# Optimization experiments

Hardware: AMD Instinct MI355X
Metric: run time of the kernel (lower is better)

The kernel has to match this reference:

```python
import jax, jax.numpy as jnp
import numpy as np

N_NODES = 50000
N_EDGES = 800000
H = 64      # node_hidden_size
S = 16      # static_feature_size
EF = 16     # edge_feature_size
ATT_IN = 2 * H + 2 * S + EF   # 176
ATT_W = 2 * H + EF            # 144
UPD_IN = 2 * H                # 128
UPD_W = 2 * H                 # 128


def setup_inputs() -> dict:
    key = jax.random.key(0)
    ks = jax.random.split(key, 12)
    x = jax.random.normal(ks[0], (N_NODES, H), dtype=jnp.float32)
    x_s = jax.random.normal(ks[1], (N_NODES, S), dtype=jnp.float32)
    edge_index = jax.random.randint(ks[2], (2, N_EDGES), 0, N_NODES, dtype=jnp.int32)
    edge_features = jax.random.normal(ks[3], (N_EDGES, EF), dtype=jnp.float32)

    def lin(k, out_dim, in_dim):
        lim = 1.0 / np.sqrt(in_dim)
        kw, kb = jax.random.split(k)
        W = jax.random.uniform(kw, (out_dim, in_dim), minval=-lim, maxval=lim, dtype=jnp.float32)
        b = jax.random.uniform(kb, (out_dim,), minval=-lim, maxval=lim, dtype=jnp.float32)
        return W, b

    att_w1, att_b1 = lin(ks[4], ATT_W, ATT_IN)
    att_w2, att_b2 = lin(ks[5], 1, ATT_W)
    upd_w1, upd_b1 = lin(ks[6], UPD_W, UPD_IN)
    upd_w2, upd_b2 = lin(ks[7], H, UPD_W)

    return {
        "x": x, "x_s": x_s, "edge_index": edge_index, "edge_features": edge_features,
        "att_w1": att_w1, "att_b1": att_b1, "att_w2": att_w2, "att_b2": att_b2,
        "upd_w1": upd_w1, "upd_b1": upd_b1, "upd_w2": upd_w2, "upd_b2": upd_b2,
    }


def segment_softmax(scores, segment_ids, num_segments):
    max_scores = jax.ops.segment_max(scores, segment_ids, num_segments=num_segments)
    exp_scores = jnp.exp(scores - max_scores[segment_ids])
    sum_exp = jax.ops.segment_sum(exp_scores, segment_ids, num_segments=num_segments)
    return exp_scores / (sum_exp[segment_ids] + 1e-9)


def reference(x, x_s, edge_index, edge_features,
              att_w1, att_b1, att_w2, att_b2,
              upd_w1, upd_b1, upd_w2, upd_b2):
    num_nodes = x.shape[0]
    src, dst = edge_index[0], edge_index[1]

    # gather per-edge features: [E, 2H+2S+EF]
    att_in = jnp.concatenate(
        [x[src], x[dst], x_s[src], x_s[dst], edge_features], axis=-1)

    # attention MLP (depth=1, relu hidden), squeeze to [E]
    h = jax.nn.relu(att_in @ att_w1.T + att_b1)
    raw = (h @ att_w2.T + att_b2).squeeze(-1)
    raw = jax.nn.leaky_relu(raw)

    attn = segment_softmax(raw, dst, num_nodes)

    # weighted scatter-sum of source hidden feats -> [N, H]
    aggregated = jax.ops.segment_sum(x[src] * attn[:, None], dst, num_segments=num_nodes)

    upd_in = jnp.concatenate([x, aggregated], axis=-1)
    u = jax.nn.relu(upd_in @ upd_w1.T + upd_b1)
    out = u @ upd_w2.T + upd_b2
    return jax.nn.relu(out)
```

## Files before the change

### kernel.cpp

```cpp
#include <hip/hip_runtime.h>
#include <math.h>

#define N_NODES_C 50000
#define E_C       800000
#define ATT_IN_C  176
#define ATT_HID_C 144
#define SCAN_B    98
#define UPD_TILES 3125

typedef __attribute__((ext_vector_type(8))) __bf16 bf16x8;
typedef __attribute__((ext_vector_type(4))) float f32x4;

#define O_RAW   0L
#define O_DEG   3201024L
#define O_OFF   3402752L
#define O_CUR   3603456L
#define O_CSR   3804160L
#define O_EFB   16605184L
#define O_XB    42206208L
#define O_XSB   48607232L
#define O_W1B   50208256L
#define O_UW1B  50259968L
#define O_UW2B  50293760L
#define O_AGGB  50311168L
#define O_PSUM  O_AGGB
#define O_BOFF  (O_AGGB + 512L)

__device__ __forceinline__ bf16x8 bzero8() {
    bf16x8 z;
#pragma unroll
    for (int i = 0; i < 8; ++i) z[i] = (__bf16)0.0f;
    return z;
}

__global__ __launch_bounds__(256) void k_deg(const int* __restrict__ ei, int* __restrict__ deg) {
    int e = blockIdx.x * blockDim.x + threadIdx.x;
    if (e < E_C) atomicAdd(&deg[ei[E_C + e]], 1);
}

__global__ __launch_bounds__(256) void k_scan1(const int* __restrict__ deg,
                                               int* __restrict__ psum) {
    __shared__ int red[256];
    int b = blockIdx.x, t = threadIdx.x;
    int i = b * 512 + t * 2;
    int s = 0;
    if (i < N_NODES_C) s += deg[i];
    if (i + 1 < N_NODES_C) s += deg[i + 1];
    red[t] = s;
    __syncthreads();
#pragma unroll
    for (int off = 128; off > 0; off >>= 1) {
        if (t < off) red[t] += red[t + off];
        __syncthreads();
    }
    if (t == 0) psum[b] = red[0];
}

__global__ __launch_bounds__(128) void k_scan2(const int* __restrict__ psum,
                                               int* __restrict__ boff,
                                               int* __restrict__ offsets) {
    __shared__ int sc[128];
    int t = threadIdx.x;
    int v = (t < SCAN_B) ? psum[t] : 0;
    sc[t] = v;
    __syncthreads();
#pragma unroll
    for (int off = 1; off < 128; off <<= 1) {
        int val = sc[t];
        int add = (t >= off) ? sc[t - off] : 0;
        __syncthreads();
        sc[t] = val + add;
        __syncthreads();
    }
    boff[t] = sc[t] - v;
    if (t == SCAN_B - 1) offsets[N_NODES_C] = sc[t];
}

__global__ __launch_bounds__(256) void k_scan3(const int* __restrict__ deg,
                                               const int* __restrict__ boff,
                                               int* __restrict__ offsets,
                                               int* __restrict__ cursor) {
    __shared__ int sc[256];
    int b = blockIdx.x, t = threadIdx.x;
    int i = b * 512 + t * 2;
    int d0 = (i < N_NODES_C) ? deg[i] : 0;
    int d1 = (i + 1 < N_NODES_C) ? deg[i + 1] : 0;
    int s = d0 + d1;
    sc[t] = s;
    __syncthreads();
#pragma unroll
    for (int off = 1; off < 256; off <<= 1) {
        int val = sc[t];
        int add = (t >= off) ? sc[t - off] : 0;
        __syncthreads();
        sc[t] = val + add;
        __syncthreads();
    }
    int excl = boff[b] + sc[t] - s;
    if (i < N_NODES_C)     { offsets[i]     = excl;      cursor[i]     = excl; }
    if (i + 1 < N_NODES_C) { offsets[i + 1] = excl + d0; cursor[i + 1] = excl + d0; }
}

__global__ __launch_bounds__(256) void k_fill(const int* __restrict__ ei,
                                              int* __restrict__ cursor,
                                              int4* __restrict__ csr) {
    int e = blockIdx.x * blockDim.x + threadIdx.x;
    if (e < E_C) {
        int src  = ei[e];
        int dst  = ei[E_C + e];
        int slot = atomicAdd(&cursor[dst], 1);
        csr[slot] = make_int4(src, dst, e, 0);
    }
}

__global__ __launch_bounds__(256) void k_cvt(
    const float* __restrict__ x, const float* __restrict__ xs,
    const float* __restrict__ ef, const float* __restrict__ w1,
    const float* __restrict__ uw1, const float* __restrict__ uw2,
    __bf16* __restrict__ xb, __bf16* __restrict__ xsb,
    __bf16* __restrict__ efb, __bf16* __restrict__ w1b,
    __bf16* __restrict__ uw1b, __bf16* __restrict__ uw2b)
{
    long g = (long)blockIdx.x * 256 + threadIdx.x;
    const long G_X = 400000, G_XS = 500000, G_EF = 2100000,
               G_W1 = 2103168, G_UW1 = 2105216, G_UW2 = 2106240;
    if (g >= G_UW2) return;
    const float* src; __bf16* dst; long off;
    if (g < G_X)        { src = x;   dst = xb;   off = g * 8; }
    else if (g < G_XS)  { src = xs;  dst = xsb;  off = (g - G_X) * 8; }
    else if (g < G_EF)  { src = ef;  dst = efb;  off = (g - G_XS) * 8; }
    else if (g < G_W1)  { src = w1;  dst = w1b;  off = (g - G_EF) * 8; }
    else if (g < G_UW1) { src = uw1; dst = uw1b; off = (g - G_W1) * 8; }
    else                { src = uw2; dst = uw2b; off = (g - G_UW1) * 8; }
    float4 a = *(const float4*)(src + off);
    float4 b = *(const float4*)(src + off + 4);
    bf16x8 o;
    o[0] = (__bf16)a.x; o[1] = (__bf16)a.y; o[2] = (__bf16)a.z; o[3] = (__bf16)a.w;
    o[4] = (__bf16)b.x; o[5] = (__bf16)b.y; o[6] = (__bf16)b.z; o[7] = (__bf16)b.w;
    *(bf16x8*)(dst + off) = o;
}

__device__ __forceinline__ void load_afrags(
    int src, int dst, int e, int quad,
    const __bf16* __restrict__ xb, const __bf16* __restrict__ xsb,
    const __bf16* __restrict__ efb,
    bf16x8 a[6])
{
    const __bf16* px = xb + (long)src * 64 + quad * 8;
    const __bf16* pd = xb + (long)dst * 64 + quad * 8;
    a[0] = *(const bf16x8*)(px);
    a[1] = *(const bf16x8*)(px + 32);
    a[2] = *(const bf16x8*)(pd);
    a[3] = *(const bf16x8*)(pd + 32);
    if (quad < 2) {
        a[4] = *(const bf16x8*)(xsb + (long)src * 16 + quad * 8);
        a[5] = *(const bf16x8*)(efb + (long)e * 16 + quad * 8);
    } else {
        a[4] = *(const bf16x8*)(xsb + (long)dst * 16 + (quad - 2) * 8);
        a[5] = bzero8();
    }
}

__global__ __launch_bounds__(256) void k_scores_mfma(
    const __bf16* __restrict__ xb, const __bf16* __restrict__ xsb,
    const __bf16* __restrict__ efb, const __bf16* __restrict__ w1b,
    const int4* __restrict__ csr,
    const float* __restrict__ b1, const float* __restrict__ w2,
    const float* __restrict__ b2, float* __restrict__ raw)
{
    int tid  = threadIdx.x;
    int lane = tid & 63;
    int w    = blockIdx.x * 4 + (tid >> 6);
    const int NP = E_C / 32;
    int per = (NP + 1023) / 1024;
    long j0 = (long)w * per;
    long j1 = j0 + per; if (j1 > NP) j1 = NP;
    if (j0 >= j1) return;

    int mrow = lane & 15;
    int quad = lane >> 4;

    bf16x8 bfr[6][9];
#pragma unroll
    for (int ks = 0; ks < 6; ++ks) {
        int k0 = ks * 32 + quad * 8;
#pragma unroll
        for (int nt = 0; nt < 9; ++nt) {
            int n = nt * 16 + mrow;
            if (k0 + 8 <= ATT_IN_C)
                bfr[ks][nt] = *(const bf16x8*)(w1b + (long)n * ATT_IN_C + k0);
            else
                bfr[ks][nt] = bzero8();
        }
    }

    float b1v[9], w2v[9];
#pragma unroll
    for (int nt = 0; nt < 9; ++nt) {
        int n = nt * 16 + mrow;
        b1v[nt] = b1[n];
        w2v[nt] = w2[n];
    }
    float b2v = b2[0];

    bf16x8 curA[6], curB[6], nxtA[6], nxtB[6];
    int4 cA = make_int4(0, 0, 0, 0), cB = cA;
    {
        int4 e0 = csr[j0 * 32 + mrow];
        int4 e1 = csr[j0 * 32 + 16 + mrow];
        load_afrags(e0.x, e0.y, e0.z, quad, xb, xsb, efb, curA);
        load_afrags(e1.x, e1.y, e1.z, quad, xb, xsb, efb, curB);
        if (j0 + 1 < j1) {
            int4 f0 = csr[(j0 + 1) * 32 + mrow];
            int4 f1 = csr[(j0 + 1) * 32 + 16 + mrow];
            load_afrags(f0.x, f0.y, f0.z, quad, xb, xsb, efb, nxtA);
            load_afrags(f1.x, f1.y, f1.z, quad, xb, xsb, efb, nxtB);
        }
    }

    for (long j = j0; j < j1; ++j) {
        if (j + 2 < j1) {
            cA = csr[(j + 2) * 32 + mrow];
            cB = csr[(j + 2) * 32 + 16 + mrow];
        }

        f32x4 accA[9], accB[9];
#pragma unroll
        for (int nt = 0; nt < 9; ++nt) {
            accA[nt] = (f32x4){0.f, 0.f, 0.f, 0.f};
            accB[nt] = (f32x4){0.f, 0.f, 0.f, 0.f};
        }

#pragma unroll
        for (int ks = 0; ks < 6; ++ks) {
#pragma unroll
            for (int nt = 0; nt < 9; ++nt) {
                accA[nt] = __builtin_amdgcn_mfma_f32_16x16x32_bf16(
                    curA[ks], bfr[ks][nt], accA[nt], 0, 0, 0);
                accB[nt] = __builtin_amdgcn_mfma_f32_16x16x32_bf16(
                    curB[ks], bfr[ks][nt], accB[nt], 0, 0, 0);
            }
        }

        float pA0 = 0.f, pA1 = 0.f, pA2 = 0.f, pA3 = 0.f;
        float pB0 = 0.f, pB1 = 0.f, pB2 = 0.f, pB3 = 0.f;
#pragma unroll
        for (int nt = 0; nt < 9; ++nt) {
            pA0 += w2v[nt] * fmaxf(accA[nt][0] + b1v[nt], 0.f);
            pA1 += w2v[nt] * fmaxf(accA[nt][1] + b1v[nt], 0.f);
            pA2 += w2v[nt] * fmaxf(accA[nt][2] + b1v[nt], 0.f);
            pA3 += w2v[nt] * fmaxf(accA[nt][3] + b1v[nt], 0.f);
            pB0 += w2v[nt] * fmaxf(accB[nt][0] + b1v[nt], 0.f);
            pB1 += w2v[nt] * fmaxf(accB[nt][1] + b1v[nt], 0.f);
            pB2 += w2v[nt] * fmaxf(accB[nt][2] + b1v[nt], 0.f);
            pB3 += w2v[nt] * fmaxf(accB[nt][3] + b1v[nt], 0.f);
        }
#pragma unroll
        for (int off = 1; off < 16; off <<= 1) {
            pA0 += __shfl_xor(pA0, off, 64);
            pA1 += __shfl_xor(pA1, off, 64);
            pA2 += __shfl_xor(pA2, off, 64);
            pA3 += __shfl_xor(pA3, off, 64);
            pB0 += __shfl_xor(pB0, off, 64);
            pB1 += __shfl_xor(pB1, off, 64);
            pB2 += __shfl_xor(pB2, off, 64);
            pB3 += __shfl_xor(pB3, off, 64);
        }
        if (mrow < 4) {
            float vA = (mrow == 0) ? pA0 : (mrow == 1) ? pA1 : (mrow == 2) ? pA2 : pA3;
            float vB = (mrow == 0) ? pB0 : (mrow == 1) ? pB1 : (mrow == 2) ? pB2 : pB3;
            vA += b2v; vB += b2v;
            vA = (vA >= 0.f) ? vA : 0.01f * vA;
            vB = (vB >= 0.f) ? vB : 0.01f * vB;
            raw[(j * 2) * 16 + quad * 4 + mrow]     = vA;
            raw[(j * 2 + 1) * 16 + quad * 4 + mrow] = vB;
        }

#pragma unroll
        for (int i = 0; i < 6; ++i) { curA[i] = nxtA[i]; curB[i] = nxtB[i]; }
        if (j + 2 < j1) {
            load_afrags(cA.x, cA.y, cA.z, quad, xb, xsb, efb, nxtA);
            load_afrags(cB.x, cB.y, cB.z, quad, xb, xsb, efb, nxtB);
        }
    }
}

__global__ __launch_bounds__(256) void k_agg(
    const __bf16* __restrict__ xb, const int* __restrict__ offsets,
    const int4* __restrict__ csr,
    const float* __restrict__ raw, __bf16* __restrict__ aggb)
{
    int tid = threadIdx.x;
    int wave = tid >> 6, lane = tid & 63;
    int v = blockIdx.x * 4 + wave;
    if (v >= N_NODES_C) return;
    int s0 = offsets[v], s1 = offsets[v + 1];

    float m = -INFINITY;
    for (int p = s0 + lane; p < s1; p += 64) m = fmaxf(m, raw[p]);
#pragma unroll
    for (int off = 32; off > 0; off >>= 1) m = fmaxf(m, __shfl_xor(m, off, 64));

    float acc = 0.f, sum = 0.f;
    for (int p = s0; p < s1; ++p) {
        int src = csr[p].x;
        float w = expf(raw[p] - m);
        sum += w;
        acc += w * (float)xb[(long)src * 64 + lane];
    }
    aggb[(long)v * 64 + lane] = (__bf16)(acc / (sum + 1e-9f));
}

__global__ __launch_bounds__(256) void k_upd_mfma(
    const __bf16* __restrict__ xb, const __bf16* __restrict__ aggb,
    const __bf16* __restrict__ w1b, const float* __restrict__ b1,
    const __bf16* __restrict__ w2b, const float* __restrict__ b2,
    float* __restrict__ out)
{
    __shared__ __bf16 ubuf[4][16 * 136];
    int tid = threadIdx.x, wid = tid >> 6, lane = tid & 63;
    int tile = blockIdx.x * 4 + wid;
    if (tile >= UPD_TILES) return;
    int mrow = lane & 15, quad = lane >> 4;

    long node = (long)tile * 16 + mrow;
    bf16x8 a1[4];
    a1[0] = *(const bf16x8*)(xb + node * 64 + quad * 8);
    a1[1] = *(const bf16x8*)(xb + node * 64 + 32 + quad * 8);
    a1[2] = *(const bf16x8*)(aggb + node * 64 + quad * 8);
    a1[3] = *(const bf16x8*)(aggb + node * 64 + 32 + quad * 8);

    bf16x8 b1f[4][8];
#pragma unroll
    for (int ks = 0; ks < 4; ++ks)
#pragma unroll
        for (int nt = 0; nt < 8; ++nt)
            b1f[ks][nt] = *(const bf16x8*)(w1b + (long)(nt * 16 + mrow) * 128 + ks * 32 + quad * 8);

    f32x4 acc1[8];
#pragma unroll
    for (int nt = 0; nt < 8; ++nt) acc1[nt] = (f32x4){0.f, 0.f, 0.f, 0.f};
#pragma unroll
    for (int ks = 0; ks < 4; ++ks)
#pragma unroll
        for (int nt = 0; nt < 8; ++nt)
            acc1[nt] = __builtin_amdgcn_mfma_f32_16x16x32_bf16(a1[ks], b1f[ks][nt], acc1[nt], 0, 0, 0);

    __bf16* ub = ubuf[wid];
#pragma unroll
    for (int nt = 0; nt < 8; ++nt) {
        float bb = b1[nt * 16 + mrow];
#pragma unroll
        for (int r = 0; r < 4; ++r) {
            float h = fmaxf(acc1[nt][r] + bb, 0.f);
            ub[(quad * 4 + r) * 136 + nt * 16 + mrow] = (__bf16)h;
        }
    }

    bf16x8 a2[4];
#pragma unroll
    for (int ks = 0; ks < 4; ++ks)
        a2[ks] = *(bf16x8*)&ub[mrow * 136 + ks * 32 + quad * 8];

    bf16x8 b2f[4][4];
#pragma unroll
    for (int ks = 0; ks < 4; ++ks)
#pragma unroll
        for (int nt = 0; nt < 4; ++nt)
            b2f[ks][nt] = *(const bf16x8*)(w2b + (long)(nt * 16 + mrow) * 128 + ks * 32 + quad * 8);

    f32x4 acc2[4];
#pragma unroll
    for (int nt = 0; nt < 4; ++nt) acc2[nt] = (f32x4){0.f, 0.f, 0.f, 0.f};
#pragma unroll
    for (int ks = 0; ks < 4; ++ks)
#pragma unroll
        for (int nt = 0; nt < 4; ++nt)
            acc2[nt] = __builtin_amdgcn_mfma_f32_16x16x32_bf16(a2[ks], b2f[ks][nt], acc2[nt], 0, 0, 0);

#pragma unroll
    for (int nt = 0; nt < 4; ++nt) {
        float bb = b2[nt * 16 + mrow];
#pragma unroll
        for (int r = 0; r < 4; ++r) {
            long nodeo = (long)tile * 16 + quad * 4 + r;
            out[nodeo * 64 + nt * 16 + mrow] = fmaxf(acc2[nt][r] + bb, 0.f);
        }
    }
}

extern "C" void kernel_launch(void* const* d_in, const int* in_sizes, int n_in,
                              void* d_out, int out_size, void* d_ws, size_t ws_size,
                              hipStream_t stream) {
    const float* x    = (const float*)d_in[0];
    const float* xs   = (const float*)d_in[1];
    const int*   ei   = (const int*)d_in[2];
    const float* ef   = (const float*)d_in[3];
    const float* aw1  = (const float*)d_in[4];
    const float* ab1  = (const float*)d_in[5];
    const float* aw2  = (const float*)d_in[6];
    const float* ab2  = (const float*)d_in[7];
    const float* uw1  = (const float*)d_in[8];
    const float* ub1  = (const float*)d_in[9];
    const float* uw2  = (const float*)d_in[10];
    const float* ub2  = (const float*)d_in[11];
    float* out = (float*)d_out;

    char* ws = (char*)d_ws;
    float*  raw     = (float*)(ws + O_RAW);
    int*    deg     = (int*)(ws + O_DEG);
    int*    offsets = (int*)(ws + O_OFF);
    int*    cursor  = (int*)(ws + O_CUR);
    int4*   csr     = (int4*)(ws + O_CSR);
    __bf16* efb     = (__bf16*)(ws + O_EFB);
    __bf16* xb      = (__bf16*)(ws + O_XB);
    __bf16* xsb     = (__bf16*)(ws + O_XSB);
    __bf16* w1b     = (__bf16*)(ws + O_W1B);
    __bf16* uw1b    = (__bf16*)(ws + O_UW1B);
    __bf16* uw2b    = (__bf16*)(ws + O_UW2B);
    __bf16* aggb    = (__bf16*)(ws + O_AGGB);
    int*    psum    = (int*)(ws + O_PSUM);
    int*    boff    = (int*)(ws + O_BOFF);

    hipMemsetAsync(deg, 0, N_NODES_C * sizeof(int), stream);
    hipLaunchKernelGGL(k_deg,      dim3((E_C + 255) / 256),       dim3(256), 0, stream, ei, deg);
    hipLaunchKernelGGL(k_scan1,    dim3(SCAN_B),                  dim3(256), 0, stream, deg, psum);
    hipLaunchKernelGGL(k_scan2,    dim3(1),                       dim3(128), 0, stream, psum, boff, offsets);
    hipLaunchKernelGGL(k_scan3,    dim3(SCAN_B),                  dim3(256), 0, stream, deg, boff, offsets, cursor);
    hipLaunchKernelGGL(k_fill,     dim3((E_C + 255) / 256),       dim3(256), 0, stream,
                       ei, cursor, csr);
    hipLaunchKernelGGL(k_cvt,      dim3(8228),                    dim3(256), 0, stream,
                       x, xs, ef, aw1, uw1, uw2, xb, xsb, efb, w1b, uw1b, uw2b);
    hipLaunchKernelGGL(k_scores_mfma, dim3(256),                  dim3(256), 0, stream,
                       xb, xsb, efb, w1b, csr, ab1, aw2, ab2, raw);
    hipLaunchKernelGGL(k_agg,      dim3((N_NODES_C + 3) / 4),     dim3(256), 0, stream,
                       xb, offsets, csr, raw, aggb);
    hipLaunchKernelGGL(k_upd_mfma, dim3((UPD_TILES + 3) / 4),     dim3(256), 0, stream,
                       xb, aggb, uw1b, ub1, uw2b, ub2, out);
}
```

Measured before the change: 400.9 us.

## Fuse degree count with conversion, merge scans, stage W1 in LDS, unroll aggregation

Merges the degree-count kernel into the bf16 conversion kernel and folds the single-block block-offset scan into the final scan kernel, which cuts two launches. The attention kernel now stages the first-layer weights in shared memory instead of holding 54 bf16x8 fragments in registers. This lowers register pressure but adds LDS reads inside the MFMA loop. The aggregation loop is unrolled by four so several gathers are in flight at once.

```diff
diff --git a/kernel.cpp b/kernel.cpp
--- a/kernel.cpp
+++ b/kernel.cpp
@@ -7,6 +7,8 @@
 #define ATT_HID_C 144
 #define SCAN_B    98
 #define UPD_TILES 3125
+#define DEG_B     3125
+#define CVT_B     8228
 
 typedef __attribute__((ext_vector_type(8))) __bf16 bf16x8;
 typedef __attribute__((ext_vector_type(4))) float f32x4;
@@ -24,7 +26,6 @@
 #define O_UW2B  50293760L
 #define O_AGGB  50311168L
 #define O_PSUM  O_AGGB
-#define O_BOFF  (O_AGGB + 512L)
 
 __device__ __forceinline__ bf16x8 bzero8() {
     bf16x8 z;
@@ -33,95 +34,23 @@
     return z;
 }
 
-__global__ __launch_bounds__(256) void k_deg(const int* __restrict__ ei, int* __restrict__ deg) {
-    int e = blockIdx.x * blockDim.x + threadIdx.x;
-    if (e < E_C) atomicAdd(&deg[ei[E_C + e]], 1);
-}
-
-__global__ __launch_bounds__(256) void k_scan1(const int* __restrict__ deg,
-                                               int* __restrict__ psum) {
-    __shared__ int red[256];
-    int b = blockIdx.x, t = threadIdx.x;
-    int i = b * 512 + t * 2;
-    int s = 0;
-    if (i < N_NODES_C) s += deg[i];
-    if (i + 1 < N_NODES_C) s += deg[i + 1];
-    red[t] = s;
-    __syncthreads();
-#pragma unroll
-    for (int off = 128; off > 0; off >>= 1) {
-        if (t < off) red[t] += red[t + off];
-        __syncthreads();
-    }
-    if (t == 0) psum[b] = red[0];
-}
-
-__global__ __launch_bounds__(128) void k_scan2(const int* __restrict__ psum,
-                                               int* __restrict__ boff,
-                                               int* __restrict__ offsets) {
-    __shared__ int sc[128];
-    int t = threadIdx.x;
-    int v = (t < SCAN_B) ? psum[t] : 0;
-    sc[t] = v;
-    __syncthreads();
-#pragma unroll
-    for (int off = 1; off < 128; off <<= 1) {
-        int val = sc[t];
-        int add = (t >= off) ? sc[t - off] : 0;
-        __syncthreads();
-        sc[t] = val + add;
-        __syncthreads();
-    }
-    boff[t] = sc[t] - v;
-    if (t == SCAN_B - 1) offsets[N_NODES_C] = sc[t];
-}
-
-__global__ __launch_bounds__(256) void k_scan3(const int* __restrict__ deg,
-                                               const int* __restrict__ boff,
-                                               int* __restrict__ offsets,
-                                               int* __restrict__ cursor) {
-    __shared__ int sc[256];
-    int b = blockIdx.x, t = threadIdx.x;
-    int i = b * 512 + t * 2;
-    int d0 = (i < N_NODES_C) ? deg[i] : 0;
-    int d1 = (i + 1 < N_NODES_C) ? deg[i + 1] : 0;
-    int s = d0 + d1;
-    sc[t] = s;
-    __syncthreads();
-#pragma unroll
-    for (int off = 1; off < 256; off <<= 1) {
-        int val = sc[t];
-        int add = (t >= off) ? sc[t - off] : 0;
-        __syncthreads();
-        sc[t] = val + add;
-        __syncthreads();
-    }
-    int excl = boff[b] + sc[t] - s;
-    if (i < N_NODES_C)     { offsets[i]     = excl;      cursor[i]     = excl; }
-    if (i + 1 < N_NODES_C) { offsets[i + 1] = excl + d0; cursor[i + 1] = excl + d0; }
-}
-
-__global__ __launch_bounds__(256) void k_fill(const int* __restrict__ ei,
-                                              int* __restrict__ cursor,
-                                              int4* __restrict__ csr) {
-    int e = blockIdx.x * blockDim.x + threadIdx.x;
-    if (e < E_C) {
-        int src  = ei[e];
-        int dst  = ei[E_C + e];
-        int slot = atomicAdd(&cursor[dst], 1);
-        csr[slot] = make_int4(src, dst, e, 0);
-    }
-}
-
-__global__ __launch_bounds__(256) void k_cvt(
+__global__ __launch_bounds__(256) void k_prep(
+    const int* __restrict__ ei,
     const float* __restrict__ x, const float* __restrict__ xs,
     const float* __restrict__ ef, const float* __restrict__ w1,
     const float* __restrict__ uw1, const float* __restrict__ uw2,
+    int* __restrict__ deg,
     __bf16* __restrict__ xb, __bf16* __restrict__ xsb,
     __bf16* __restrict__ efb, __bf16* __restrict__ w1b,
     __bf16* __restrict__ uw1b, __bf16* __restrict__ uw2b)
 {
-    long g = (long)blockIdx.x * 256 + threadIdx.x;
+    int bid = blockIdx.x;
+    if (bid < DEG_B) {
+        int e = bid * 256 + threadIdx.x;
+        if (e < E_C) atomicAdd(&deg[ei[E_C + e]], 1);
+        return;
+    }
+    long g = (long)(bid - DEG_B) * 256 + threadIdx.x;
     const long G_X = 400000, G_XS = 500000, G_EF = 2100000,
                G_W1 = 2103168, G_UW1 = 2105216, G_UW2 = 2106240;
     if (g >= G_UW2) return;
@@ -138,6 +67,75 @@
     o[0] = (__bf16)a.x; o[1] = (__bf16)a.y; o[2] = (__bf16)a.z; o[3] = (__bf16)a.w;
     o[4] = (__bf16)b.x; o[5] = (__bf16)b.y; o[6] = (__bf16)b.z; o[7] = (__bf16)b.w;
     *(bf16x8*)(dst + off) = o;
+}
+
+__global__ __launch_bounds__(256) void k_scan1(const int* __restrict__ deg,
+                                               int* __restrict__ psum) {
+    __shared__ int red[256];
+    int b = blockIdx.x, t = threadIdx.x;
+    int i = b * 512 + t * 2;
+    int s = 0;
+    if (i < N_NODES_C) s += deg[i];
+    if (i + 1 < N_NODES_C) s += deg[i + 1];
+    red[t] = s;
+    __syncthreads();
+#pragma unroll
+    for (int off = 128; off > 0; off >>= 1) {
+        if (t < off) red[t] += red[t + off];
+        __syncthreads();
+    }
+    if (t == 0) psum[b] = red[0];
+}
+
+__global__ __launch_bounds__(256) void k_scan3(const int* __restrict__ deg,
+                                               const int* __restrict__ psum,
+                                               int* __restrict__ offsets,
+                                               int* __restrict__ cursor) {
+    __shared__ int sc[256];
+    __shared__ int bo[2];
+    int b = blockIdx.x, t = threadIdx.x;
+    if (t < 64) {
+        int v1 = (t < SCAN_B) ? psum[t] : 0;
+        int v2 = (t + 64 < SCAN_B) ? psum[t + 64] : 0;
+        int c   = ((t < b) ? v1 : 0) + ((t + 64 < b) ? v2 : 0);
+        int tot = v1 + v2;
+#pragma unroll
+        for (int off = 32; off > 0; off >>= 1) {
+            c   += __shfl_xor(c, off, 64);
+            tot += __shfl_xor(tot, off, 64);
+        }
+        if (t == 0) { bo[0] = c; bo[1] = tot; }
+    }
+    int i = b * 512 + t * 2;
+    int d0 = (i < N_NODES_C) ? deg[i] : 0;
+    int d1 = (i + 1 < N_NODES_C) ? deg[i + 1] : 0;
+    int s = d0 + d1;
+    sc[t] = s;
+    __syncthreads();
+#pragma unroll
+    for (int off = 1; off < 256; off <<= 1) {
+        int val = sc[t];
+        int add = (t >= off) ? sc[t - off] : 0;
+        __syncthreads();
+        sc[t] = val + add;
+        __syncthreads();
+    }
+    int excl = bo[0] + sc[t] - s;
+    if (i < N_NODES_C)     { offsets[i]     = excl;      cursor[i]     = excl; }
+    if (i + 1 < N_NODES_C) { offsets[i + 1] = excl + d0; cursor[i + 1] = excl + d0; }
+    if (b == 0 && t == 0)  offsets[N_NODES_C] = bo[1];
+}
+
+__global__ __launch_bounds__(256) void k_fill(const int* __restrict__ ei,
+                                              int* __restrict__ cursor,
+                                              int4* __restrict__ csr) {
+    int e = blockIdx.x * blockDim.x + threadIdx.x;
+    if (e < E_C) {
+        int src  = ei[e];
+        int dst  = ei[E_C + e];
+        int slot = atomicAdd(&cursor[dst], 1);
+        csr[slot] = make_int4(src, dst, e, 0);
+    }
 }
 
 __device__ __forceinline__ void load_afrags(
@@ -168,9 +166,19 @@
     const float* __restrict__ b1, const float* __restrict__ w2,
     const float* __restrict__ b2, float* __restrict__ raw)
 {
+    __shared__ __bf16 w1s[144 * 184];
     int tid  = threadIdx.x;
     int lane = tid & 63;
-    int w    = blockIdx.x * 4 + (tid >> 6);
+
+    for (int c = tid; c < 144 * 22; c += 256) {
+        int n = c / 22, kk = (c % 22) * 8;
+        *(bf16x8*)&w1s[n * 184 + kk] = *(const bf16x8*)(w1b + (long)n * ATT_IN_C + kk);
+    }
+    for (int n = tid; n < 144; n += 256)
+        *(bf16x8*)&w1s[n * 184 + 176] = bzero8();
+    __syncthreads();
+
+    int w = blockIdx.x * 4 + (tid >> 6);
     const int NP = E_C / 32;
     int per = (NP + 1023) / 1024;
     long j0 = (long)w * per;
@@ -179,20 +187,7 @@
 
     int mrow = lane & 15;
     int quad = lane >> 4;
-
-    bf16x8 bfr[6][9];
-#pragma unroll
-    for (int ks = 0; ks < 6; ++ks) {
-        int k0 = ks * 32 + quad * 8;
-#pragma unroll
-        for (int nt = 0; nt < 9; ++nt) {
-            int n = nt * 16 + mrow;
-            if (k0 + 8 <= ATT_IN_C)
-                bfr[ks][nt] = *(const bf16x8*)(w1b + (long)n * ATT_IN_C + k0);
-            else
-                bfr[ks][nt] = bzero8();
-        }
-    }
+    const __bf16* wls = &w1s[mrow * 184 + quad * 8];
 
     float b1v[9], w2v[9];
 #pragma unroll
@@ -235,10 +230,11 @@
         for (int ks = 0; ks < 6; ++ks) {
 #pragma unroll
             for (int nt = 0; nt < 9; ++nt) {
+                bf16x8 bf = *(const bf16x8*)(wls + nt * (16 * 184) + ks * 32);
                 accA[nt] = __builtin_amdgcn_mfma_f32_16x16x32_bf16(
-                    curA[ks], bfr[ks][nt], accA[nt], 0, 0, 0);
+                    curA[ks], bf, accA[nt], 0, 0, 0);
                 accB[nt] = __builtin_amdgcn_mfma_f32_16x16x32_bf16(
-                    curB[ks], bfr[ks][nt], accB[nt], 0, 0, 0);
+                    curB[ks], bf, accB[nt], 0, 0, 0);
             }
         }
 
@@ -302,7 +298,20 @@
     for (int off = 32; off > 0; off >>= 1) m = fmaxf(m, __shfl_xor(m, off, 64));
 
     float acc = 0.f, sum = 0.f;
-    for (int p = s0; p < s1; ++p) {
+    int p = s0;
+    for (; p + 4 <= s1; p += 4) {
+        int4 c0 = csr[p], c1 = csr[p + 1], c2 = csr[p + 2], c3 = csr[p + 3];
+        float r0 = raw[p], r1 = raw[p + 1], r2 = raw[p + 2], r3 = raw[p + 3];
+        float v0 = (float)xb[(long)c0.x * 64 + lane];
+        float v1 = (float)xb[(long)c1.x * 64 + lane];
+        float v2 = (float)xb[(long)c2.x * 64 + lane];
+        float v3 = (float)xb[(long)c3.x * 64 + lane];
+        float w0 = expf(r0 - m), w1 = expf(r1 - m);
+        float w2 = expf(r2 - m), w3 = expf(r3 - m);
+        sum += (w0 + w1) + (w2 + w3);
+        acc += w0 * v0 + w1 * v1 + w2 * v2 + w3 * v3;
+    }
+    for (; p < s1; ++p) {
         int src = csr[p].x;
         float w = expf(raw[p] - m);
         sum += w;
@@ -420,17 +429,15 @@
     __bf16* uw2b    = (__bf16*)(ws + O_UW2B);
     __bf16* aggb    = (__bf16*)(ws + O_AGGB);
     int*    psum    = (int*)(ws + O_PSUM);
-    int*    boff    = (int*)(ws + O_BOFF);
 
     hipMemsetAsync(deg, 0, N_NODES_C * sizeof(int), stream);
-    hipLaunchKernelGGL(k_deg,      dim3((E_C + 255) / 256),       dim3(256), 0, stream, ei, deg);
+    hipLaunchKernelGGL(k_prep,     dim3(DEG_B + CVT_B),           dim3(256), 0, stream,
+                       ei, x, xs, ef, aw1, uw1, uw2, deg, xb, xsb, efb, w1b, uw1b, uw2b);
     hipLaunchKernelGGL(k_scan1,    dim3(SCAN_B),                  dim3(256), 0, stream, deg, psum);
-    hipLaunchKernelGGL(k_scan2,    dim3(1),                       dim3(128), 0, stream, psum, boff, offsets);
-    hipLaunchKernelGGL(k_scan3,    dim3(SCAN_B),                  dim3(256), 0, stream, deg, boff, offsets, cursor);
+    hipLaunchKernelGGL(k_scan3,    dim3(SCAN_B),                  dim3(256), 0, stream,
+                       deg, psum, offsets, cursor);
     hipLaunchKernelGGL(k_fill,     dim3((E_C + 255) / 256),       dim3(256), 0, stream,
                        ei, cursor, csr);
-    hipLaunchKernelGGL(k_cvt,      dim3(8228),                    dim3(256), 0, stream,
-                       x, xs, ef, aw1, uw1, uw2, xb, xsb, efb, w1b, uw1b, uw2b);
     hipLaunchKernelGGL(k_scores_mfma, dim3(256),                  dim3(256), 0, stream,
                        xb, xsb, efb, w1b, csr, ab1, aw2, ab2, raw);
     hipLaunchKernelGGL(k_agg,      dim3((N_NODES_C + 3) / 4),     dim3(256), 0, stream,
```

Measured after the change: 354.9 us. 11.5% less time.
